# Optimization experiments

Measured on AMD Instinct MI355X. Metric: run time of the kernel, lower is better.

Reference implementation:

```python
import jax, jax.numpy as jnp
import numpy as np

K = 7          # kernel_size
STRIDE = 1
GC = 4         # group_channels (fixed in module)
BN_EPS = 1e-5


def setup_inputs() -> dict:
    key = jax.random.key(0)
    ks = jax.random.split(key, 4)
    B, C, H, W = 4, 256, 56, 56
    Cr = C // 4              # reduction_ratio = 4
    G = C // GC              # groups = 64
    K2 = K * K               # 49
    x = jax.random.normal(ks[0], (B, C, H, W), jnp.float32)
    w1 = jax.random.normal(ks[1], (Cr, C), jnp.float32) * 0.05   # conv1 1x1
    b1 = jnp.zeros((Cr,), jnp.float32)
    gamma = jnp.ones((Cr,), jnp.float32)
    beta = jnp.zeros((Cr,), jnp.float32)
    bn_mean = jnp.zeros((Cr,), jnp.float32)
    bn_var = jnp.ones((Cr,), jnp.float32)
    w2 = jax.random.normal(ks[2], (K2 * G, Cr), jnp.float32) * 0.05  # conv2 1x1
    b2 = jnp.zeros((K2 * G,), jnp.float32)
    return {"x": x, "w1": w1, "b1": b1, "gamma": gamma, "beta": beta,
            "bn_mean": bn_mean, "bn_var": bn_var, "w2": w2, "b2": b2}


def reference(x, w1, b1, gamma, beta, bn_mean, bn_var, w2, b2):
    B, C, H, W = x.shape
    G = C // GC
    K2 = K * K
    p = (K - 1) // 2

    # kernel-generation branch (stride == 1 -> no avgpool)
    y = jnp.einsum('oc,bchw->bohw', w1, x) + b1[None, :, None, None]
    # BatchNorm (inference, running stats)
    inv = gamma / jnp.sqrt(bn_var + BN_EPS)
    y = y * inv[None, :, None, None] + (beta - bn_mean * inv)[None, :, None, None]
    y = jax.nn.relu(y)
    weight = jnp.einsum('oc,bchw->bohw', w2, y) + b2[None, :, None, None]
    Ho, Wo = weight.shape[2], weight.shape[3]
    weight = weight.reshape(B, G, K2, Ho, Wo)

    # unfold: zero-pad then gather k*k shifted views (channel-major like torch Unfold)
    xp = jnp.pad(x, ((0, 0), (0, 0), (p, p), (p, p)))
    patches = jnp.stack(
        [xp[:, :, i:i + H:STRIDE, j:j + W:STRIDE] for i in range(K) for j in range(K)],
        axis=2)                                    # (B, C, K2, Ho, Wo)
    patches = patches.reshape(B, G, GC, K2, Ho, Wo)

    # per-pixel dynamic kernel multiply-accumulate over k^2
    out = jnp.einsum('bgkhw,bgckhw->bgchw', weight, patches)
    return out.reshape(B, C, Ho, Wo)
```

## Files before the change

kernel.cpp:

```cpp
#include <hip/hip_runtime.h>
#include <hip/hip_fp16.h>

typedef _Float16 h8 __attribute__((ext_vector_type(8)));
typedef _Float16 h2v __attribute__((ext_vector_type(2)));
typedef __fp16 fp16x2 __attribute__((ext_vector_type(2)));
typedef float f32x4 __attribute__((ext_vector_type(4)));

#define HW 3136
#define NPX 12544
#define YSTR 96
#define XROW 16
#define XSEG 148
#define PS2 456
#define WGT_W 3648
#define W2R 3584

union UH { unsigned int u; h2v h; fp16x2 p; };
__device__ __forceinline__ h2v uh(unsigned int u) { UH v; v.u = u; return v.h; }
__device__ __forceinline__ unsigned int hu(h2v h) { UH v; v.h = h; return v.u; }
#define BLO(w) __builtin_shufflevector(w, w, 0, 0)
#define BHI(w) __builtin_shufflevector(w, w, 1, 1)

__device__ __forceinline__ unsigned int pkrtz(float a, float b) {
    UH v; v.p = __builtin_amdgcn_cvt_pkrtz(a, b); return v.u;
}
__device__ __forceinline__ unsigned short f2hu(float f) {
    union { __half h; unsigned short u; } v; v.h = __float2half(f); return v.u;
}
__device__ __forceinline__ float fget(const float4& v, int e) {
    return e == 0 ? v.x : e == 1 ? v.y : e == 2 ? v.z : v.w;
}

__global__ __launch_bounds__(256) void kyw(
    const float* __restrict__ x, const float* __restrict__ w1,
    const float* __restrict__ b1, const float* __restrict__ gamma,
    const float* __restrict__ beta, const float* __restrict__ mean,
    const float* __restrict__ var, const float* __restrict__ w2,
    const float* __restrict__ b2, unsigned short* __restrict__ ytb,
    unsigned short* __restrict__ w2b96)
{
    __shared__ unsigned short xt[16 * 264];
    const int t = threadIdx.x, bid = blockIdx.x;

    if (bid >= 784) {
        const int r0 = (bid - 784) * 16;
#pragma unroll
        for (int i = 0; i < 6; ++i) {
            int j = i * 256 + t;
            int row = r0 + j / 96, col = j - (j / 96) * 96;
            int c8 = row / 448, rem = row - c8 * 448;
            int g = rem / 56, s = rem - g * 56;
            int ki = s >> 3, kj = s & 7;
            float v = 0.f;
            if (kj < 7) {
                int o = (c8 * 8 + g) * 49 + ki * 7 + kj;
                v = col < 64 ? w2[o * 64 + col] : (col == 64 ? b2[o] : 0.f);
            }
            w2b96[row * 96 + col] = f2hu(v);
        }
        return;
    }

    const int px0 = bid * 16;
    const int b = px0 / HW;
    const int p0 = px0 - b * HW;

#pragma unroll
    for (int i = 0; i < 4; ++i) {
        int j = i * 256 + t;
        int c = j >> 2, pq = j & 3;
        float4 v = *(const float4*)(x + (size_t)(b * 256 + c) * HW + p0 + pq * 4);
        xt[(pq * 4 + 0) * 264 + c] = f2hu(v.x);
        xt[(pq * 4 + 1) * 264 + c] = f2hu(v.y);
        xt[(pq * 4 + 2) * 264 + c] = f2hu(v.z);
        xt[(pq * 4 + 3) * 264 + c] = f2hu(v.w);
    }
    if (t < 16) {
        unsigned short* yr = ytb + (size_t)(px0 + t) * YSTR + 64;
        ushort4 one; one.x = 0x3C00u; one.y = 0; one.z = 0; one.w = 0;
        ushort4 z; z.x = 0; z.y = 0; z.z = 0; z.w = 0;
        *(ushort4*)(yr) = one;
#pragma unroll
        for (int q = 1; q < 8; ++q) *(ushort4*)(yr + q * 4) = z;
    }
    __syncthreads();

    const int lane = t & 63, wave = t >> 6;
    const int n = lane & 15, quad = lane >> 4;
    const int m0 = wave * 16;

    f32x4 acc = {0.f, 0.f, 0.f, 0.f};
#pragma unroll
    for (int k = 0; k < 8; ++k) {
        const float* wrow = w1 + (m0 + n) * 256 + k * 32 + quad * 8;
        float4 wa = *(const float4*)(wrow);
        float4 wb = *(const float4*)(wrow + 4);
        union { uint4 u; h8 h; } A;
        A.u.x = pkrtz(wa.x, wa.y);
        A.u.y = pkrtz(wa.z, wa.w);
        A.u.z = pkrtz(wb.x, wb.y);
        A.u.w = pkrtz(wb.z, wb.w);
        h8 bfv = *(const h8*)(&xt[n * 264 + k * 32 + quad * 8]);
        acc = __builtin_amdgcn_mfma_f32_16x16x32_f16(A.h, bfv, acc, 0, 0, 0);
    }
    float pv[4];
#pragma unroll
    for (int r = 0; r < 4; ++r) {
        int m = m0 + quad * 4 + r;
        float sc = gamma[m] * rsqrtf(var[m] + 1e-5f);
        float sh = beta[m] - mean[m] * sc + b1[m] * sc;
        pv[r] = fmaxf(acc[r] * sc + sh, 0.f);
    }
    uint2 pk;
    pk.x = pkrtz(pv[0], pv[1]);
    pk.y = pkrtz(pv[2], pv[3]);
    *(uint2*)(ytb + (size_t)(px0 + n) * YSTR + m0 + quad * 4) = pk;
}

__global__ __launch_bounds__(256, 6) void kmain(
    const float* __restrict__ x, const unsigned short* __restrict__ w2b96,
    const unsigned short* __restrict__ ytb, float* __restrict__ out)
{
    __shared__ __align__(16) unsigned int smem_u[WGT_W + 16 * XSEG];
    unsigned short* wgt16 = (unsigned short*)smem_u;
    unsigned int* xsb = smem_u + WGT_W;

    const int t = threadIdx.x;
    const int pix = t & 15, sub = t >> 4;
    const int lane = t & 63, wave = t >> 6;
    const int bc = blockIdx.x;
    const int b = bc >> 3, c8 = bc & 7;
    const int w0 = blockIdx.y * 8, h0 = blockIdx.z * 2;
    const int ph = pix >> 3, pw = pix & 7;
    const int h = h0 + ph, w = w0 + pw;
    const int n = lane & 15, quad = lane >> 4;

    const int Pn = b * HW + (h0 + (n >> 3)) * 56 + w0 + (n & 7);
    const unsigned short* yrp = ytb + (size_t)Pn * YSTR + quad * 8;
    const h8 bf0 = *(const h8*)(yrp);
    const h8 bf1 = *(const h8*)(yrp + 32);
    const h8 bf2 = *(const h8*)(yrp + 64);

    if (t < 128) {
        const int seg = t & 15, jr = t >> 4;
        const int jg = seg >> 1, jcp = seg & 1;
        const int hh = h0 + jr - 3;
        const bool rowok = (hh >= 0) && (hh < 56);
        const float* src = x + ((size_t)b * 256 + c8 * 32 + jg * 4 + jcp * 2) * HW + hh * 56;
        float4 va[2][4];
#pragma unroll
        for (int q = 0; q < 4; ++q) {
            int col0 = w0 - 4 + q * 4;
            bool ok = rowok && (col0 >= 0) && (col0 <= 52);
#pragma unroll
            for (int ci = 0; ci < 2; ++ci)
                va[ci][q] = ok ? *(const float4*)(src + ci * HW + col0)
                              : make_float4(0.f, 0.f, 0.f, 0.f);
        }
        unsigned int* dst = xsb + seg * XSEG + jr * XROW;
#pragma unroll
        for (int q = 0; q < 4; ++q)
#pragma unroll
            for (int e = 0; e < 4; ++e) {
                int c = q * 4 + e - 1;
                if (c >= 0 && c < 14)
                    dst[c] = pkrtz(fget(va[0][q], e), fget(va[1][q], e));
            }
    }

    const int c0 = c8 * 448;
    for (int tile = wave; tile < 28; tile += 4) {
        const unsigned short* ap = w2b96 + (size_t)(c0 + tile * 16 + n) * 96 + quad * 8;
        h8 af0 = *(const h8*)(ap);
        h8 af1 = *(const h8*)(ap + 32);
        h8 af2 = *(const h8*)(ap + 64);
        f32x4 acc = {0.f, 0.f, 0.f, 0.f};
        acc = __builtin_amdgcn_mfma_f32_16x16x32_f16(af0, bf0, acc, 0, 0, 0);
        acc = __builtin_amdgcn_mfma_f32_16x16x32_f16(af1, bf1, acc, 0, 0, 0);
        acc = __builtin_amdgcn_mfma_f32_16x16x32_f16(af2, bf2, acc, 0, 0, 0);
        uint2 pk2;
        pk2.x = pkrtz(acc[0], acc[1]);
        pk2.y = pkrtz(acc[2], acc[3]);
        *(uint2*)(wgt16 + n * PS2 + tile * 16 + quad * 4) = pk2;
    }
    __syncthreads();

    const int g = sub & 7, cp = sub >> 3;
    const unsigned short* wr16 = wgt16 + pix * PS2 + g * 56;
    const unsigned int* xr = xsb + (g * 2 + cp) * XSEG + ph * XROW + pw;
    h2v acA = {(_Float16)0.f, (_Float16)0.f};
    h2v acB = acA;
#pragma unroll
    for (int ki = 0; ki < 7; ++ki) {
        uint4 wq = *(const uint4*)(wr16 + ki * 8);
        const unsigned int* xrow = xr + ki * XROW;
        unsigned int xv[7];
#pragma unroll
        for (int j = 0; j < 7; ++j) xv[j] = xrow[j];
        h2v w01 = uh(wq.x), w23 = uh(wq.y), w45 = uh(wq.z), w6p = uh(wq.w);
        acA += BLO(w01) * uh(xv[0]);
        acB += BHI(w01) * uh(xv[1]);
        acA += BLO(w23) * uh(xv[2]);
        acB += BHI(w23) * uh(xv[3]);
        acA += BLO(w45) * uh(xv[4]);
        acB += BHI(w45) * uh(xv[5]);
        acA += BLO(w6p) * uh(xv[6]);
    }
    h2v acc2 = acA + acB;
    float a0 = (float)acc2[0];
    float a1 = (float)acc2[1];

    size_t ob = ((size_t)b * 256 + c8 * 32 + g * 4 + cp * 2) * HW + h * 56 + w;
    out[ob] = a0;
    out[ob + HW] = a1;
}

extern "C" void kernel_launch(void* const* d_in, const int* in_sizes, int n_in,
                              void* d_out, int out_size, void* d_ws, size_t ws_size,
                              hipStream_t stream) {
    const float* x     = (const float*)d_in[0];
    const float* w1    = (const float*)d_in[1];
    const float* b1    = (const float*)d_in[2];
    const float* gamma = (const float*)d_in[3];
    const float* beta  = (const float*)d_in[4];
    const float* mean  = (const float*)d_in[5];
    const float* var   = (const float*)d_in[6];
    const float* w2    = (const float*)d_in[7];
    const float* b2    = (const float*)d_in[8];
    float* out = (float*)d_out;

    unsigned short* ytb   = (unsigned short*)d_ws;
    unsigned short* w2b96 = ytb + (size_t)NPX * YSTR;
    hipLaunchKernelGGL(kyw, dim3(1008), dim3(256), 0, stream,
                       x, w1, b1, gamma, beta, mean, var, w2, b2, ytb, w2b96);
    hipLaunchKernelGGL(kmain, dim3(32, 7, 28), dim3(256), 0, stream,
                       x, w2b96, ytb, out);
}
```

Measured before the change: 139.1 us.

## Fuse conv1+BN+ReLU into main kernel, recomputing per-tile y in LDS

Removes the separate pass that computed the reduced feature map y for every pixel and stored it to global memory. Each main-kernel block now loads its 16 pixels across all 256 channels, converts them to fp16 in LDS and runs the conv1 MFMA there, using a BN-prescaled fp16 w1 and a shift vector prepared by a small prep kernel. This drops the y write/read round trip and most of the first kernel's work. In exchange, each of the 8 channel-group blocks for a pixel tile recomputes the same y, which means extra x reads (mostly from cache), more LDS use and an extra barrier.

After: 160.1 us. 15.1% more time.

```diff
diff --git a/kernel.cpp b/kernel.cpp
--- a/kernel.cpp
+++ b/kernel.cpp
@@ -7,13 +7,13 @@
 typedef float f32x4 __attribute__((ext_vector_type(4)));
 
 #define HW 3136
-#define NPX 12544
-#define YSTR 96
 #define XROW 16
 #define XSEG 148
 #define PS2 456
 #define WGT_W 3648
-#define W2R 3584
+#define XSB_W 2368
+#define YB_W  768
+#define SMEM_W (WGT_W + XSB_W + YB_W)
 
 union UH { unsigned int u; h2v h; fp16x2 p; };
 __device__ __forceinline__ h2v uh(unsigned int u) { UH v; v.u = u; return v.h; }
@@ -31,99 +31,56 @@
     return e == 0 ? v.x : e == 1 ? v.y : e == 2 ? v.z : v.w;
 }
 
-__global__ __launch_bounds__(256) void kyw(
-    const float* __restrict__ x, const float* __restrict__ w1,
-    const float* __restrict__ b1, const float* __restrict__ gamma,
-    const float* __restrict__ beta, const float* __restrict__ mean,
-    const float* __restrict__ var, const float* __restrict__ w2,
-    const float* __restrict__ b2, unsigned short* __restrict__ ytb,
-    unsigned short* __restrict__ w2b96)
+__global__ __launch_bounds__(256) void kprep(
+    const float* __restrict__ w1, const float* __restrict__ b1,
+    const float* __restrict__ gamma, const float* __restrict__ beta,
+    const float* __restrict__ mean, const float* __restrict__ var,
+    const float* __restrict__ w2, const float* __restrict__ b2,
+    unsigned short* __restrict__ w2b96, unsigned short* __restrict__ w1h,
+    float* __restrict__ sh2)
 {
-    __shared__ unsigned short xt[16 * 264];
     const int t = threadIdx.x, bid = blockIdx.x;
-
-    if (bid >= 784) {
-        const int r0 = (bid - 784) * 16;
-#pragma unroll
-        for (int i = 0; i < 6; ++i) {
+    if (bid == 224) {
+#pragma unroll
+        for (int i = 0; i < 64; ++i) {
             int j = i * 256 + t;
-            int row = r0 + j / 96, col = j - (j / 96) * 96;
-            int c8 = row / 448, rem = row - c8 * 448;
-            int g = rem / 56, s = rem - g * 56;
-            int ki = s >> 3, kj = s & 7;
-            float v = 0.f;
-            if (kj < 7) {
-                int o = (c8 * 8 + g) * 49 + ki * 7 + kj;
-                v = col < 64 ? w2[o * 64 + col] : (col == 64 ? b2[o] : 0.f);
-            }
-            w2b96[row * 96 + col] = f2hu(v);
+            int row = j >> 8;
+            float sc = gamma[row] * rsqrtf(var[row] + 1e-5f);
+            w1h[j] = f2hu(w1[j] * sc);
+        }
+        if (t < 64) {
+            float sc = gamma[t] * rsqrtf(var[t] + 1e-5f);
+            sh2[t] = beta[t] - mean[t] * sc + b1[t] * sc;
         }
         return;
     }
-
-    const int px0 = bid * 16;
-    const int b = px0 / HW;
-    const int p0 = px0 - b * HW;
-
-#pragma unroll
-    for (int i = 0; i < 4; ++i) {
+    const int r0 = bid * 16;
+#pragma unroll
+    for (int i = 0; i < 6; ++i) {
         int j = i * 256 + t;
-        int c = j >> 2, pq = j & 3;
-        float4 v = *(const float4*)(x + (size_t)(b * 256 + c) * HW + p0 + pq * 4);
-        xt[(pq * 4 + 0) * 264 + c] = f2hu(v.x);
-        xt[(pq * 4 + 1) * 264 + c] = f2hu(v.y);
-        xt[(pq * 4 + 2) * 264 + c] = f2hu(v.z);
-        xt[(pq * 4 + 3) * 264 + c] = f2hu(v.w);
-    }
-    if (t < 16) {
-        unsigned short* yr = ytb + (size_t)(px0 + t) * YSTR + 64;
-        ushort4 one; one.x = 0x3C00u; one.y = 0; one.z = 0; one.w = 0;
-        ushort4 z; z.x = 0; z.y = 0; z.z = 0; z.w = 0;
-        *(ushort4*)(yr) = one;
-#pragma unroll
-        for (int q = 1; q < 8; ++q) *(ushort4*)(yr + q * 4) = z;
-    }
-    __syncthreads();
-
-    const int lane = t & 63, wave = t >> 6;
-    const int n = lane & 15, quad = lane >> 4;
-    const int m0 = wave * 16;
-
-    f32x4 acc = {0.f, 0.f, 0.f, 0.f};
-#pragma unroll
-    for (int k = 0; k < 8; ++k) {
-        const float* wrow = w1 + (m0 + n) * 256 + k * 32 + quad * 8;
-        float4 wa = *(const float4*)(wrow);
-        float4 wb = *(const float4*)(wrow + 4);
-        union { uint4 u; h8 h; } A;
-        A.u.x = pkrtz(wa.x, wa.y);
-        A.u.y = pkrtz(wa.z, wa.w);
-        A.u.z = pkrtz(wb.x, wb.y);
-        A.u.w = pkrtz(wb.z, wb.w);
-        h8 bfv = *(const h8*)(&xt[n * 264 + k * 32 + quad * 8]);
-        acc = __builtin_amdgcn_mfma_f32_16x16x32_f16(A.h, bfv, acc, 0, 0, 0);
-    }
-    float pv[4];
-#pragma unroll
-    for (int r = 0; r < 4; ++r) {
-        int m = m0 + quad * 4 + r;
-        float sc = gamma[m] * rsqrtf(var[m] + 1e-5f);
-        float sh = beta[m] - mean[m] * sc + b1[m] * sc;
-        pv[r] = fmaxf(acc[r] * sc + sh, 0.f);
-    }
-    uint2 pk;
-    pk.x = pkrtz(pv[0], pv[1]);
-    pk.y = pkrtz(pv[2], pv[3]);
-    *(uint2*)(ytb + (size_t)(px0 + n) * YSTR + m0 + quad * 4) = pk;
+        int row = r0 + j / 96, col = j - (j / 96) * 96;
+        int c8 = row / 448, rem = row - c8 * 448;
+        int g = rem / 56, s = rem - g * 56;
+        int ki = s >> 3, kj = s & 7;
+        float v = 0.f;
+        if (kj < 7) {
+            int o = (c8 * 8 + g) * 49 + ki * 7 + kj;
+            v = col < 64 ? w2[o * 64 + col] : (col == 64 ? b2[o] : 0.f);
+        }
+        w2b96[row * 96 + col] = f2hu(v);
+    }
 }
 
 __global__ __launch_bounds__(256, 6) void kmain(
     const float* __restrict__ x, const unsigned short* __restrict__ w2b96,
-    const unsigned short* __restrict__ ytb, float* __restrict__ out)
+    const unsigned short* __restrict__ w1h, const float* __restrict__ sh2,
+    float* __restrict__ out)
 {
-    __shared__ __align__(16) unsigned int smem_u[WGT_W + 16 * XSEG];
+    __shared__ __align__(16) unsigned int smem_u[SMEM_W];
     unsigned short* wgt16 = (unsigned short*)smem_u;
+    unsigned short* xt = (unsigned short*)smem_u;
     unsigned int* xsb = smem_u + WGT_W;
+    unsigned short* yb = (unsigned short*)(smem_u + WGT_W + XSB_W);
 
     const int t = threadIdx.x;
     const int pix = t & 15, sub = t >> 4;
@@ -135,18 +92,26 @@
     const int h = h0 + ph, w = w0 + pw;
     const int n = lane & 15, quad = lane >> 4;
 
-    const int Pn = b * HW + (h0 + (n >> 3)) * 56 + w0 + (n & 7);
-    const unsigned short* yrp = ytb + (size_t)Pn * YSTR + quad * 8;
-    const h8 bf0 = *(const h8*)(yrp);
-    const h8 bf1 = *(const h8*)(yrp + 32);
-    const h8 bf2 = *(const h8*)(yrp + 64);
+    const float* xb = x + (size_t)b * 256 * HW;
+#pragma unroll
+    for (int i = 0; i < 4; ++i) {
+        int j = i * 256 + t;
+        int c = j >> 2, pq = j & 3;
+        int row = h0 + (pq >> 1), col = w0 + (pq & 1) * 4;
+        float4 v = *(const float4*)(xb + (size_t)c * HW + row * 56 + col);
+        int p = (pq >> 1) * 8 + (pq & 1) * 4;
+        xt[(p + 0) * 264 + c] = f2hu(v.x);
+        xt[(p + 1) * 264 + c] = f2hu(v.y);
+        xt[(p + 2) * 264 + c] = f2hu(v.z);
+        xt[(p + 3) * 264 + c] = f2hu(v.w);
+    }
 
     if (t < 128) {
         const int seg = t & 15, jr = t >> 4;
         const int jg = seg >> 1, jcp = seg & 1;
         const int hh = h0 + jr - 3;
         const bool rowok = (hh >= 0) && (hh < 56);
-        const float* src = x + ((size_t)b * 256 + c8 * 32 + jg * 4 + jcp * 2) * HW + hh * 56;
+        const float* src = xb + ((size_t)c8 * 32 + jg * 4 + jcp * 2) * HW + hh * 56;
         float4 va[2][4];
 #pragma unroll
         for (int q = 0; q < 4; ++q) {
@@ -168,20 +133,53 @@
             }
     }
 
-    const int c0 = c8 * 448;
-    for (int tile = wave; tile < 28; tile += 4) {
-        const unsigned short* ap = w2b96 + (size_t)(c0 + tile * 16 + n) * 96 + quad * 8;
-        h8 af0 = *(const h8*)(ap);
-        h8 af1 = *(const h8*)(ap + 32);
-        h8 af2 = *(const h8*)(ap + 64);
+    if (t < 16) {
+        unsigned short* yr = yb + t * 96 + 64;
+        ushort4 one; one.x = 0x3C00u; one.y = 0; one.z = 0; one.w = 0;
+        ushort4 z; z.x = 0; z.y = 0; z.z = 0; z.w = 0;
+        *(ushort4*)(yr) = one;
+#pragma unroll
+        for (int q = 1; q < 8; ++q) *(ushort4*)(yr + q * 4) = z;
+    }
+    __syncthreads();
+
+    {
+        const int m0 = wave * 16;
         f32x4 acc = {0.f, 0.f, 0.f, 0.f};
-        acc = __builtin_amdgcn_mfma_f32_16x16x32_f16(af0, bf0, acc, 0, 0, 0);
-        acc = __builtin_amdgcn_mfma_f32_16x16x32_f16(af1, bf1, acc, 0, 0, 0);
-        acc = __builtin_amdgcn_mfma_f32_16x16x32_f16(af2, bf2, acc, 0, 0, 0);
-        uint2 pk2;
-        pk2.x = pkrtz(acc[0], acc[1]);
-        pk2.y = pkrtz(acc[2], acc[3]);
-        *(uint2*)(wgt16 + n * PS2 + tile * 16 + quad * 4) = pk2;
+#pragma unroll
+        for (int k = 0; k < 8; ++k) {
+            h8 aw = *(const h8*)(w1h + (size_t)(m0 + n) * 256 + k * 32 + quad * 8);
+            h8 bv = *(const h8*)(&xt[n * 264 + k * 32 + quad * 8]);
+            acc = __builtin_amdgcn_mfma_f32_16x16x32_f16(aw, bv, acc, 0, 0, 0);
+        }
+        float4 shv = *(const float4*)(sh2 + m0 + quad * 4);
+        uint2 pk;
+        pk.x = pkrtz(fmaxf(acc[0] + shv.x, 0.f), fmaxf(acc[1] + shv.y, 0.f));
+        pk.y = pkrtz(fmaxf(acc[2] + shv.z, 0.f), fmaxf(acc[3] + shv.w, 0.f));
+        *(uint2*)(yb + n * 96 + m0 + quad * 4) = pk;
+    }
+    __syncthreads();
+
+    {
+        const unsigned short* yrp = yb + n * 96 + quad * 8;
+        const h8 bf0 = *(const h8*)(yrp);
+        const h8 bf1 = *(const h8*)(yrp + 32);
+        const h8 bf2 = *(const h8*)(yrp + 64);
+        const int c0 = c8 * 448;
+        for (int tile = wave; tile < 28; tile += 4) {
+            const unsigned short* ap = w2b96 + (size_t)(c0 + tile * 16 + n) * 96 + quad * 8;
+            h8 af0 = *(const h8*)(ap);
+            h8 af1 = *(const h8*)(ap + 32);
+            h8 af2 = *(const h8*)(ap + 64);
+            f32x4 acc = {0.f, 0.f, 0.f, 0.f};
+            acc = __builtin_amdgcn_mfma_f32_16x16x32_f16(af0, bf0, acc, 0, 0, 0);
+            acc = __builtin_amdgcn_mfma_f32_16x16x32_f16(af1, bf1, acc, 0, 0, 0);
+            acc = __builtin_amdgcn_mfma_f32_16x16x32_f16(af2, bf2, acc, 0, 0, 0);
+            uint2 pk2;
+            pk2.x = pkrtz(acc[0], acc[1]);
+            pk2.y = pkrtz(acc[2], acc[3]);
+            *(uint2*)(wgt16 + n * PS2 + tile * 16 + quad * 4) = pk2;
+        }
     }
     __syncthreads();
 
@@ -229,10 +227,12 @@
     const float* b2    = (const float*)d_in[8];
     float* out = (float*)d_out;
 
-    unsigned short* ytb   = (unsigned short*)d_ws;
-    unsigned short* w2b96 = ytb + (size_t)NPX * YSTR;
-    hipLaunchKernelGGL(kyw, dim3(1008), dim3(256), 0, stream,
-                       x, w1, b1, gamma, beta, mean, var, w2, b2, ytb, w2b96);
+    unsigned short* w2b96 = (unsigned short*)d_ws;
+    unsigned short* w1h   = w2b96 + (size_t)3584 * 96;
+    float* sh2            = (float*)(w1h + 16384);
+
+    hipLaunchKernelGGL(kprep, dim3(225), dim3(256), 0, stream,
+                       w1, b1, gamma, beta, mean, var, w2, b2, w2b96, w1h, sh2);
     hipLaunchKernelGGL(kmain, dim3(32, 7, 28), dim3(256), 0, stream,
-                       x, w2b96, ytb, out);
-}
+                       x, w2b96, w1h, sh2, out);
+}
```
